# Kernel tuning notes

Hardware: AMD Instinct MI355X
Metric: run time of the kernel (lower is better)

Reference implementation:

```python
import jax, jax.numpy as jnp
import numpy as np

GRID_SIZE = 5
SPLINE_ORDER = 3
GRID_RANGE = (-1.0, 1.0)


def b_splines(x, grid, spline_order=SPLINE_ORDER):
    # x: [B, in], grid: [G] with G = grid_size + 2*spline_order + 1
    x = x[..., None]                      # [B, in, 1]
    g = grid[None, None, :]               # [1, 1, G]
    bases = ((x >= g[..., :-1]) & (x < g[..., 1:])).astype(x.dtype)  # [B, in, G-1]
    for k in range(1, spline_order + 1):
        left = (x - g[..., :-(k + 1)]) / (g[..., k:-1] - g[..., :-(k + 1)]) * bases[..., :-1]
        right = (g[..., k + 1:] - x) / (g[..., k + 1:] - g[..., 1:-k]) * bases[..., 1:]
        bases = left + right
    return bases                          # [B, in, grid_size + spline_order]


def setup_inputs() -> dict:
    key = jax.random.key(0)
    k1, k2, k3, k4 = jax.random.split(key, 4)
    B, IN, OUT = 32768, 256, 256
    n_coef = GRID_SIZE + SPLINE_ORDER  # 8
    h = (GRID_RANGE[1] - GRID_RANGE[0]) / GRID_SIZE
    grid = jnp.arange(-SPLINE_ORDER, GRID_SIZE + SPLINE_ORDER + 1, dtype=jnp.float32) * h + GRID_RANGE[0]  # [12]
    x = jax.random.normal(k1, (B, IN), dtype=jnp.float32)
    base_weight = jax.random.normal(k2, (OUT, IN), dtype=jnp.float32) * np.sqrt(2.0 / IN)
    spline_weight = jax.random.normal(k3, (OUT, IN, n_coef), dtype=jnp.float32) * (0.1 / GRID_SIZE)
    spline_scaler = jax.random.normal(k4, (OUT, IN), dtype=jnp.float32) * np.sqrt(2.0 / IN)
    return {"x": x, "base_weight": base_weight, "spline_weight": spline_weight,
            "spline_scaler": spline_scaler, "grid": grid}


def reference(x, base_weight, spline_weight, spline_scaler, grid):
    B = x.shape[0]
    out_features = base_weight.shape[0]
    # base branch: silu(x) @ base_weight^T
    base_out = jnp.matmul(jax.nn.silu(x), base_weight.T)  # [B, out]
    # spline branch
    bases = b_splines(x, grid)                             # [B, in, n_coef]
    scaled_w = spline_weight * spline_scaler[..., None]    # [out, in, n_coef]
    spline_out = jnp.matmul(bases.reshape(B, -1), scaled_w.reshape(out_features, -1).T)
    return base_out + spline_out
```

## Files before the change

### kernel.cpp

```cpp
#include <hip/hip_runtime.h>
#include <stdint.h>


#define IN_F 256
#define OUT_F 256
#define KDIM 2304
#define BK 64
#define NCHUNK (KDIM / BK)
#define TBINS 512
#define NTAB (11 * TBINS)
#define NTAB_PAD (NTAB + 2)
#define WC_BYTES ((size_t)OUT_F * KDIM * 2)

#define AS1 __attribute__((address_space(1)))
#define AS3 __attribute__((address_space(3)))

typedef float f32x4 __attribute__((ext_vector_type(4)));
typedef short bf16x8 __attribute__((ext_vector_type(8)));

__device__ __forceinline__ uint32_t f2bf(float f) {
    union { float f; uint32_t u; } c; c.f = f;
    uint32_t u = c.u;
    return (u + 0x7FFFu + ((u >> 16) & 1u)) >> 16;
}

__device__ __forceinline__ float silu_f(float v) {
    return v / (1.0f + __expf(-v));
}

__global__ void build_w(const float* __restrict__ bw, const float* __restrict__ sw,
                        const float* __restrict__ ss, unsigned short* __restrict__ Wc,
                        uint4* __restrict__ tgt) {
    const int o = blockIdx.x;
    const int i = threadIdx.x;
    Wc[o * KDIM + i] = (unsigned short)f2bf(bw[o * IN_F + i]);
    const float scal = ss[o * IN_F + i];
    const float4* swv = reinterpret_cast<const float4*>(sw + (size_t)(o * IN_F + i) * 8);
    float4 s0 = swv[0], s1 = swv[1];
    uint4 wv;
    wv.x = f2bf(s0.x * scal) | (f2bf(s0.y * scal) << 16);
    wv.y = f2bf(s0.z * scal) | (f2bf(s0.w * scal) << 16);
    wv.z = f2bf(s1.x * scal) | (f2bf(s1.y * scal) << 16);
    wv.w = f2bf(s1.z * scal) | (f2bf(s1.w * scal) << 16);
    *reinterpret_cast<uint4*>(Wc + o * KDIM + IN_F + i * 8) = wv;

    if (o == 0) {
        for (int e = i; e < NTAB_PAD; e += IN_F) {
            uint32_t h[4] = {0u, 0u, 0u, 0u};
            if (e >= 1 && e <= NTAB) {
                const int idx = e - 1;
                const int j0 = idx >> 9;
                const float t = ((idx & (TBINS - 1)) + 0.5f) * (1.0f / TBINS);
                const float t2 = t * t, t3 = t2 * t;
                float p[4];
                p[3] = t3 * (1.0f / 6.0f);
                p[2] = -0.5f * t3 + 0.5f * t2 + 0.5f * t + (1.0f / 6.0f);
                p[1] = 0.5f * t3 - t2 + (2.0f / 3.0f);
                const float omt = 1.0f - t;
                p[0] = omt * omt * omt * (1.0f / 6.0f);
#pragma unroll
                for (int m = 0; m < 4; ++m) {
                    int c = j0 - 3 + m;
                    if (c >= 0 && c < 8) h[c >> 1] |= f2bf(p[m]) << ((c & 1) * 16);
                }
            }
            uint4 e4; e4.x = h[0]; e4.y = h[1]; e4.z = h[2]; e4.w = h[3];
            tgt[e] = e4;
        }
    }
}

__launch_bounds__(1024, 4)
__global__ void kan_fused(const float* __restrict__ x, const unsigned short* __restrict__ Wc,
                          const uint4* __restrict__ tgt, float* __restrict__ out) {
    extern __shared__ __align__(16) unsigned short smem[];
    unsigned short* const Asb = smem;
    unsigned short* const Bsb = smem + 2 * 128 * 64;

    const int bid = blockIdx.x;
    const int row0 = bid * 128;
    const int tid = threadIdx.x;
    const int lane = tid & 63;
    const int w = tid >> 6;
    const int wm = w >> 2;
    const int wn = w & 3;
    const int l15 = lane & 15;
    const int q = lane >> 4;

    const int sr = lane >> 3;
    const int s  = lane & 7;
    const int g  = s ^ sr;
    const int arow = w * 8 + sr;
    const int brow = w * 16 + sr;

    f32x4 acc[2][4] = {};
    float xr[8];
    uint4 pk;

    auto stage_b = [&](int kc, int buf) {
#pragma unroll
        for (int j = 0; j < 2; ++j) {
            const unsigned short* gp =
                Wc + (size_t)(brow + j * 8) * KDIM + kc * BK + g * 8;
            __builtin_amdgcn_global_load_lds((const AS1 void*)gp,
                (AS3 void*)(Bsb + buf * (256 * 64) + (w * 16 + j * 8) * 64), 16, 0, 0);
        }
    };
    auto load_x = [&](int kc) {
        if (kc < 4) {
            const float* xp = x + (size_t)(row0 + arow) * IN_F + kc * 64 + g * 8;
            float4 a = *reinterpret_cast<const float4*>(xp);
            float4 b = *reinterpret_cast<const float4*>(xp + 4);
            xr[0] = a.x; xr[1] = a.y; xr[2] = a.z; xr[3] = a.w;
            xr[4] = b.x; xr[5] = b.y; xr[6] = b.z; xr[7] = b.w;
        } else {
            const int i0 = (kc - 4) * 8 + g;
            float xx = x[(size_t)(row0 + arow) * IN_F + i0];
            float u = __builtin_fmaf(xx, 2.5f, 5.5f);
            int ic = (int)floorf(u * (float)TBINS);
            ic = ic < -1 ? -1 : (ic > NTAB ? NTAB : ic);
            pk = tgt[ic + 1];
        }
    };
    auto write_a = [&](int kc, int buf) {
        uint4 wv;
        if (kc < 4) {
            wv.x = f2bf(silu_f(xr[0])) | (f2bf(silu_f(xr[1])) << 16);
            wv.y = f2bf(silu_f(xr[2])) | (f2bf(silu_f(xr[3])) << 16);
            wv.z = f2bf(silu_f(xr[4])) | (f2bf(silu_f(xr[5])) << 16);
            wv.w = f2bf(silu_f(xr[6])) | (f2bf(silu_f(xr[7])) << 16);
        } else {
            wv = pk;
        }
        *reinterpret_cast<uint4*>(Asb + buf * (128 * 64) + arow * 64 + s * 8) = wv;
    };

    stage_b(0, 0);
    load_x(0);
    write_a(0, 0);
    __syncthreads();

    for (int kc = 0; kc < NCHUNK; ++kc) {
        const int cur = kc & 1;
        const int nxt = cur ^ 1;
        if (kc + 1 < NCHUNK) {
            stage_b(kc + 1, nxt);
            load_x(kc + 1);
        }
        const unsigned short* Ac = Asb + cur * (128 * 64);
        const unsigned short* Bc = Bsb + cur * (256 * 64);
#pragma unroll
        for (int kk = 0; kk < BK; kk += 32) {
            bf16x8 af[2], bfv[4];
            const int g0 = (kk >> 3) + q;
#pragma unroll
            for (int mt = 0; mt < 2; ++mt) {
                int r = wm * 32 + mt * 16 + l15;
                af[mt] = *reinterpret_cast<const bf16x8*>(
                    Ac + r * 64 + ((g0 ^ (r & 7)) << 3));
            }
#pragma unroll
            for (int nt = 0; nt < 4; ++nt) {
                int r = wn * 64 + nt * 16 + l15;
                bfv[nt] = *reinterpret_cast<const bf16x8*>(
                    Bc + r * 64 + ((g0 ^ (r & 7)) << 3));
            }
#pragma unroll
            for (int mt = 0; mt < 2; ++mt)
#pragma unroll
                for (int nt = 0; nt < 4; ++nt)
                    acc[mt][nt] = __builtin_amdgcn_mfma_f32_16x16x32_bf16(
                        af[mt], bfv[nt], acc[mt][nt], 0, 0, 0);
        }
        if (kc + 1 < NCHUNK) write_a(kc + 1, nxt);
        __syncthreads();
    }

#pragma unroll
    for (int mt = 0; mt < 2; ++mt) {
        int row = row0 + wm * 32 + mt * 16 + q * 4;
#pragma unroll
        for (int nt = 0; nt < 4; ++nt) {
            int col = wn * 64 + nt * 16 + l15;
#pragma unroll
            for (int r = 0; r < 4; ++r)
                out[(size_t)(row + r) * OUT_F + col] = acc[mt][nt][r];
        }
    }
}

extern "C" void kernel_launch(void* const* d_in, const int* in_sizes, int n_in,
                              void* d_out, int out_size, void* d_ws, size_t ws_size,
                              hipStream_t stream) {
    const float* x  = (const float*)d_in[0];
    const float* bw = (const float*)d_in[1];
    const float* sw = (const float*)d_in[2];
    const float* ss = (const float*)d_in[3];
    unsigned short* Wc = (unsigned short*)d_ws;
    uint4* tgt = (uint4*)((char*)d_ws + WC_BYTES);

    static bool attr_set = false;
    if (!attr_set) {
        (void)hipFuncSetAttribute(reinterpret_cast<const void*>(kan_fused),
                                  hipFuncAttributeMaxDynamicSharedMemorySize,
                                  96 * 1024);
        attr_set = true;
    }

    build_w<<<dim3(OUT_F), dim3(IN_F), 0, stream>>>(bw, sw, ss, Wc, tgt);

    const int B_ROWS = in_sizes[0] / IN_F;
    kan_fused<<<dim3(B_ROWS / 128), dim3(1024), 96 * 1024, stream>>>(
        x, Wc, tgt, (float*)d_out);
}
```

Measured before the change: 146.7 us.

## Shrink block tile to 64 rows with 512 threads and prefetch two chunks ahead

The fused GEMM block tile changes from 128x256 to 64x256 rows with 512 threads, which doubles the grid size and cuts LDS use to 80KB, presumably so more blocks fit per CU. Each wave now stages 32 rows of the B tile. The x loads are double-registered (even/odd) so loads run two chunks ahead, and the MFMA sections are wrapped in s_setprio to raise wave priority while issuing matrix ops. In exchange, every B tile is reloaded from global/L2 twice as often overall, so weight reuse per block is halved.

```diff
diff --git a/kernel.cpp b/kernel.cpp
--- a/kernel.cpp
+++ b/kernel.cpp
@@ -11,6 +11,7 @@
 #define NTAB (11 * TBINS)
 #define NTAB_PAD (NTAB + 2)
 #define WC_BYTES ((size_t)OUT_F * KDIM * 2)
+#define LDS_BYTES (80 * 1024)
 
 #define AS1 __attribute__((address_space(1)))
 #define AS3 __attribute__((address_space(3)))
@@ -70,15 +71,15 @@
     }
 }
 
-__launch_bounds__(1024, 4)
+__launch_bounds__(512, 4)
 __global__ void kan_fused(const float* __restrict__ x, const unsigned short* __restrict__ Wc,
                           const uint4* __restrict__ tgt, float* __restrict__ out) {
     extern __shared__ __align__(16) unsigned short smem[];
     unsigned short* const Asb = smem;
-    unsigned short* const Bsb = smem + 2 * 128 * 64;
+    unsigned short* const Bsb = smem + 2 * 64 * 64;
 
     const int bid = blockIdx.x;
-    const int row0 = bid * 128;
+    const int row0 = bid * 64;
     const int tid = threadIdx.x;
     const int lane = tid & 63;
     const int w = tid >> 6;
@@ -91,30 +92,30 @@
     const int s  = lane & 7;
     const int g  = s ^ sr;
     const int arow = w * 8 + sr;
-    const int brow = w * 16 + sr;
+    const int brow = w * 32 + sr;
 
     f32x4 acc[2][4] = {};
-    float xr[8];
-    uint4 pk;
+    float xrE[8], xrO[8];
+    uint4 pkE, pkO;
 
     auto stage_b = [&](int kc, int buf) {
 #pragma unroll
-        for (int j = 0; j < 2; ++j) {
+        for (int j = 0; j < 4; ++j) {
             const unsigned short* gp =
                 Wc + (size_t)(brow + j * 8) * KDIM + kc * BK + g * 8;
             __builtin_amdgcn_global_load_lds((const AS1 void*)gp,
-                (AS3 void*)(Bsb + buf * (256 * 64) + (w * 16 + j * 8) * 64), 16, 0, 0);
-        }
-    };
-    auto load_x = [&](int kc) {
-        if (kc < 4) {
-            const float* xp = x + (size_t)(row0 + arow) * IN_F + kc * 64 + g * 8;
+                (AS3 void*)(Bsb + buf * (256 * 64) + (w * 32 + j * 8) * 64), 16, 0, 0);
+        }
+    };
+    auto load_x = [&](int c, float* xr, uint4& pk) {
+        if (c < 4) {
+            const float* xp = x + (size_t)(row0 + arow) * IN_F + c * 64 + g * 8;
             float4 a = *reinterpret_cast<const float4*>(xp);
             float4 b = *reinterpret_cast<const float4*>(xp + 4);
             xr[0] = a.x; xr[1] = a.y; xr[2] = a.z; xr[3] = a.w;
             xr[4] = b.x; xr[5] = b.y; xr[6] = b.z; xr[7] = b.w;
         } else {
-            const int i0 = (kc - 4) * 8 + g;
+            const int i0 = (c - 4) * 8 + g;
             float xx = x[(size_t)(row0 + arow) * IN_F + i0];
             float u = __builtin_fmaf(xx, 2.5f, 5.5f);
             int ic = (int)floorf(u * (float)TBINS);
@@ -122,9 +123,9 @@
             pk = tgt[ic + 1];
         }
     };
-    auto write_a = [&](int kc, int buf) {
+    auto write_a = [&](int c, int buf, const float* xr, const uint4& pk) {
         uint4 wv;
-        if (kc < 4) {
+        if (c < 4) {
             wv.x = f2bf(silu_f(xr[0])) | (f2bf(silu_f(xr[1])) << 16);
             wv.y = f2bf(silu_f(xr[2])) | (f2bf(silu_f(xr[3])) << 16);
             wv.z = f2bf(silu_f(xr[4])) | (f2bf(silu_f(xr[5])) << 16);
@@ -132,22 +133,10 @@
         } else {
             wv = pk;
         }
-        *reinterpret_cast<uint4*>(Asb + buf * (128 * 64) + arow * 64 + s * 8) = wv;
-    };
-
-    stage_b(0, 0);
-    load_x(0);
-    write_a(0, 0);
-    __syncthreads();
-
-    for (int kc = 0; kc < NCHUNK; ++kc) {
-        const int cur = kc & 1;
-        const int nxt = cur ^ 1;
-        if (kc + 1 < NCHUNK) {
-            stage_b(kc + 1, nxt);
-            load_x(kc + 1);
-        }
-        const unsigned short* Ac = Asb + cur * (128 * 64);
+        *reinterpret_cast<uint4*>(Asb + buf * (64 * 64) + arow * 64 + s * 8) = wv;
+    };
+    auto mfma_block = [&](int cur) {
+        const unsigned short* Ac = Asb + cur * (64 * 64);
         const unsigned short* Bc = Bsb + cur * (256 * 64);
 #pragma unroll
         for (int kk = 0; kk < BK; kk += 32) {
@@ -165,15 +154,38 @@
                 bfv[nt] = *reinterpret_cast<const bf16x8*>(
                     Bc + r * 64 + ((g0 ^ (r & 7)) << 3));
             }
+            __builtin_amdgcn_s_setprio(1);
 #pragma unroll
             for (int mt = 0; mt < 2; ++mt)
 #pragma unroll
                 for (int nt = 0; nt < 4; ++nt)
                     acc[mt][nt] = __builtin_amdgcn_mfma_f32_16x16x32_bf16(
                         af[mt], bfv[nt], acc[mt][nt], 0, 0, 0);
-        }
-        if (kc + 1 < NCHUNK) write_a(kc + 1, nxt);
-        __syncthreads();
+            __builtin_amdgcn_s_setprio(0);
+        }
+    };
+
+    stage_b(0, 0);
+    load_x(0, xrE, pkE);
+    write_a(0, 0, xrE, pkE);
+    load_x(1, xrO, pkO);
+    __syncthreads();
+
+    for (int kc = 0; kc < NCHUNK; kc += 2) {
+        {
+            if (kc + 1 < NCHUNK) stage_b(kc + 1, 1);
+            if (kc + 2 < NCHUNK) load_x(kc + 2, xrE, pkE);
+            mfma_block(0);
+            if (kc + 1 < NCHUNK) write_a(kc + 1, 1, xrO, pkO);
+            __syncthreads();
+        }
+        {
+            if (kc + 2 < NCHUNK) stage_b(kc + 2, 0);
+            if (kc + 3 < NCHUNK) load_x(kc + 3, xrO, pkO);
+            mfma_block(1);
+            if (kc + 2 < NCHUNK) write_a(kc + 2, 0, xrE, pkE);
+            __syncthreads();
+        }
     }
 
 #pragma unroll
@@ -203,13 +215,13 @@
     if (!attr_set) {
         (void)hipFuncSetAttribute(reinterpret_cast<const void*>(kan_fused),
                                   hipFuncAttributeMaxDynamicSharedMemorySize,
-                                  96 * 1024);
+                                  LDS_BYTES);
         attr_set = true;
     }
 
     build_w<<<dim3(OUT_F), dim3(IN_F), 0, stream>>>(bw, sw, ss, Wc, tgt);
 
     const int B_ROWS = in_sizes[0] / IN_F;
-    kan_fused<<<dim3(B_ROWS / 128), dim3(1024), 96 * 1024, stream>>>(
+    kan_fused<<<dim3(B_ROWS / 64), dim3(512), LDS_BYTES, stream>>>(
         x, Wc, tgt, (float*)d_out);
 }
```

Result: no change. 145.5 us (-0.8%).
